# Optimization experiments

Hardware: AMD Instinct MI355X
Metric: run time of the kernel (lower is better)

The kernel has to match this reference:

```python
import jax, jax.numpy as jnp
import numpy as np

DIM = 1024
HEAD_DIM = 64
NUM_HEADS = DIM // HEAD_DIM
SCALE = HEAD_DIM ** -0.5
B, N, M = 2, 1024, 2048


def setup_inputs() -> dict:
    key = jax.random.key(0)
    ks = jax.random.split(key, 7)
    x = jax.random.normal(ks[0], (B, N, DIM), dtype=jnp.float32)
    context = jax.random.normal(ks[1], (B, M, DIM), dtype=jnp.float32)
    # query row has at least one valid key (avoids all -inf softmax rows).
    mask = jax.random.bernoulli(ks[2], 0.9, (B, N, M))
    mask = mask.at[:, :, 0].set(True)
    # Linear params (torch nn.Linear convention: y = x @ W.T + b)
    sq = (1.0 / DIM) ** 0.5
    Wq = jax.random.uniform(ks[3], (DIM, DIM), minval=-sq, maxval=sq, dtype=jnp.float32)
    Wkv = jax.random.uniform(ks[4], (2 * DIM, DIM), minval=-sq, maxval=sq, dtype=jnp.float32)
    b_kv = jax.random.uniform(ks[5], (2 * DIM,), minval=-sq, maxval=sq, dtype=jnp.float32)
    Wo = jax.random.uniform(ks[6], (DIM, DIM), minval=-sq, maxval=sq, dtype=jnp.float32)
    return {"x": x, "context": context, "mask": mask,
            "Wq": Wq, "Wkv": Wkv, "b_kv": b_kv, "Wo": Wo}


def reference(x, context, mask, Wq, Wkv, b_kv, Wo):
    b, n, c = x.shape
    m = context.shape[1]
    h, d = NUM_HEADS, HEAD_DIM
    # Q projection (no bias): [b, n, h, d] -> bhnd
    q = (x @ Wq.T).reshape(b, n, h, d).transpose(0, 2, 1, 3)
    # KV projection (with bias): [b, m, 2, h, d]
    kv = (context @ Wkv.T + b_kv).reshape(b, m, 2, h, d)
    k = kv[:, :, 0].transpose(0, 2, 1, 3)  # bhmd
    v = kv[:, :, 1].transpose(0, 2, 1, 3)  # bhmd
    # scores: bhnm, scale applied after matmul as in the original
    attn = jnp.einsum('bhnd,bhmd->bhnm', q, k) * SCALE
    attn = jnp.where(mask[:, None, :, :], attn, -jnp.inf)
    attn = jax.nn.softmax(attn, axis=-1)
    out = jnp.einsum('bhnm,bhmd->bhnd', attn, v)
    out = out.transpose(0, 2, 1, 3).reshape(b, n, h * d)
    return out @ Wo.T
```

## Files before the change

### kernel.cpp

```cpp
#include <hip/hip_runtime.h>


typedef __attribute__((ext_vector_type(8))) short short8;
typedef __attribute__((ext_vector_type(4))) short short4v;
typedef __attribute__((ext_vector_type(4))) float f32x4;
typedef __attribute__((ext_vector_type(4))) int int4v;

#define SCL2E 0.18033688011112042592f

__device__ __forceinline__ short f2bf(float f) {
  unsigned u = __float_as_uint(f);
  u += 0x7fffu + ((u >> 16) & 1u);
  return (short)(u >> 16);
}
__device__ __forceinline__ int cvt_pk_bf16(float a, float b) {
  int r;
  asm("v_cvt_pk_bf16_f32 %0, %1, %2" : "=v"(r) : "v"(a), "v"(b));
  return r;
}
__device__ __forceinline__ void gld_lds16(const void* gp, void* lp) {
  __builtin_amdgcn_global_load_lds(
      (const __attribute__((address_space(1))) unsigned int*)gp,
      (__attribute__((address_space(3))) unsigned int*)lp, 16, 0, 0);
}
__device__ __forceinline__ void sbar() {
  __builtin_amdgcn_sched_barrier(0);
  __builtin_amdgcn_s_barrier();
  __builtin_amdgcn_sched_barrier(0);
}
#define WAITVM(N) asm volatile("s_waitcnt vmcnt(" #N ")" ::: "memory")

__device__ __forceinline__ void pipesync() {
  asm volatile("s_waitcnt vmcnt(0) lgkmcnt(0)" ::: "memory");
  __builtin_amdgcn_sched_barrier(0);
  __builtin_amdgcn_s_barrier();
  __builtin_amdgcn_sched_barrier(0);
}
__device__ __forceinline__ short4v cvt4(float4 v) {
  short4v o;
  o[0] = f2bf(v.x); o[1] = f2bf(v.y); o[2] = f2bf(v.z); o[3] = f2bf(v.w);
  return o;
}
__device__ __forceinline__ size_t off64(int row, int k) {
  return ((size_t)(((row >> 6) * 32 + (k >> 5)) * 4 + ((row >> 4) & 3)) << 9) +
         (((((k >> 3) & 3) * 16 + (row & 15)) << 3) + (k & 7));
}

__global__ __launch_bounds__(256) void prep(
    const unsigned char* __restrict__ mask, unsigned long long* __restrict__ pm,
    const float* __restrict__ Wq, const float* __restrict__ Wkv,
    const float* __restrict__ Wo, const float* __restrict__ x,
    const float* __restrict__ ctx, short* __restrict__ wqb,
    short* __restrict__ wkvb, short* __restrict__ wob,
    short* __restrict__ xb, short* __restrict__ ctxb) {
  __shared__ __align__(16) short lds[64][136];
  const int row = blockIdx.x;
  const int wave = threadIdx.x >> 6, lane = threadIdx.x & 63;
  const unsigned char p8 = mask[lane * 4 + 1];
  const int p32 = ((const int*)mask)[lane * 2 + 1];
  const int shift =
      (__ballot(p8 != 0) != 0ull) ? 0 : ((__ballot(p32 != 0) != 0ull) ? 2 : 3);
  const size_t mbase = ((size_t)row * 2048) << shift;
#pragma unroll
  for (int j = 0; j < 8; j++) {
    const int c = wave * 512 + j * 64 + lane;
    const unsigned long long bits = __ballot(mask[mbase + ((size_t)c << shift)] != 0);
    if (lane == 0) pm[(size_t)row * 32 + wave * 8 + j] = bits;
  }

  const int bid = blockIdx.x;
  if (bid >= 1280) return;
  const float* src;
  short* dst;
  int cb;
  bool t64 = false;
  if (bid < 256) {
    src = x; dst = xb; cb = bid;
  } else if (bid < 768) {
    src = ctx; dst = ctxb; cb = bid - 256;
  } else if (bid < 1024) {
    src = Wkv; dst = wkvb; cb = bid - 768;
  } else if (bid < 1152) {
    src = Wq; dst = wqb; cb = bid - 1024;
  } else {
    src = Wo; dst = wob; cb = bid - 1152; t64 = true;
  }
  const int R0 = (cb >> 3) * 64, C0 = (cb & 7) * 128;
  const int t = threadIdx.x;
#pragma unroll
  for (int p = 0; p < 8; p++) {
    const int r = R0 + p * 8 + (t >> 5), c = C0 + (t & 31) * 4;
    const float4 v = *(const float4*)(src + (size_t)r * 1024 + c);
    *(short4v*)&lds[p * 8 + (t >> 5)][(t & 31) * 4] = cvt4(v);
  }
  __syncthreads();
  const int rt = t64 ? (R0 >> 6) : (R0 >> 7);
  const int f0 = t64 ? 0 : ((R0 >> 6) & 1) * 4;
  const int fl = t >> 6, q = (t >> 4) & 3, r15 = t & 15;
  const int lrow = fl * 16 + r15;
#pragma unroll
  for (int kc_l = 0; kc_l < 4; kc_l++) {
    const int kc = (C0 >> 5) + kc_l;
    const size_t base = t64 ? ((size_t)((rt * 32 + kc) * 4)) * 512
                            : ((size_t)((rt * 32 + kc) * 8 + f0)) * 512;
    const short8 vv = *(const short8*)&lds[lrow][kc_l * 32 + q * 8];
    *(short8*)(dst + base + t * 8) = vv;
  }
}

__global__ __launch_bounds__(256, 3)
void qkv_gemm(const short* __restrict__ xb, const short* __restrict__ ctxb,
              const short* __restrict__ wqb, const short* __restrict__ wkvb,
              const float* __restrict__ bias, short* __restrict__ qws,
              short* __restrict__ kws, short* __restrict__ vtws) {
  __shared__ __align__(16) short ldsA[3][4096];
  __shared__ __align__(16) short ldsB[3][4096];
  const int tid = threadIdx.x;
  const int wave = tid >> 6, lane = tid & 63;
  const int l15 = lane & 15, lg = lane >> 4;
  const int bx0 = blockIdx.x;
  const int bx = (bx0 & 7) * 80 + (bx0 >> 3);
  const bool isKV = bx < 512;
  const int rt = isKV ? (bx >> 4) : ((bx - 512) >> 3);
  const int ct = isKV ? (bx & 15) : ((bx - 512) & 7);
  const short* Amat = isKV ? ctxb : xb;
  const short* Bw = isKV ? wkvb : wqb;
  const int wr = wave >> 1, wc = wave & 1;

  f32x4 acc[4][4];
#pragma unroll
  for (int i = 0; i < 4; i++)
#pragma unroll
    for (int j = 0; j < 4; j++) acc[i][j] = (f32x4){0.f, 0.f, 0.f, 0.f};

  const short* ga0 = Amat + (size_t)rt * 131072 + wave * 512 + lane * 8;
  const short* ga1 = ga0 + 2048;
  const short* gb0 = Bw + (size_t)ct * 131072 + wave * 512 + lane * 8;
  const short* gb1 = gb0 + 2048;

  auto stage = [&](int kk, int buf) {
    const size_t koff = (size_t)kk * 4096;
    short* dA = &ldsA[buf][0];
    short* dB = &ldsB[buf][0];
    gld_lds16(ga0 + koff, dA + wave * 512);
    gld_lds16(ga1 + koff, dA + (wave + 4) * 512);
    gld_lds16(gb0 + koff, dB + wave * 512);
    gld_lds16(gb1 + koff, dB + (wave + 4) * 512);
  };
  auto compute = [&](int buf) {
    const short* sA = &ldsA[buf][0];
    const short* sB = &ldsB[buf][0];
    short8 af[4], bfr[4];
#pragma unroll
    for (int t = 0; t < 4; t++)
      af[t] = *(const short8*)&sA[((wr * 4 + t) * 64 + lane) * 8];
#pragma unroll
    for (int t = 0; t < 4; t++)
      bfr[t] = *(const short8*)&sB[((wc * 4 + t) * 64 + lane) * 8];
#pragma unroll
    for (int i = 0; i < 4; i++)
#pragma unroll
      for (int j = 0; j < 4; j++)
        acc[i][j] =
            __builtin_amdgcn_mfma_f32_16x16x32_bf16(af[i], bfr[j], acc[i][j], 0, 0, 0);
  };

  stage(0, 0);
  stage(1, 1);
  int cur = 0, nxt = 2;
  for (int i = 0; i < 30; ++i) {
    WAITVM(4);
    sbar();
    stage(i + 2, nxt);
    compute(cur);
    cur = (cur == 2) ? 0 : cur + 1;
    nxt = (nxt == 2) ? 0 : nxt + 1;
  }
  WAITVM(4);
  sbar();
  compute(cur);
  cur = (cur == 2) ? 0 : cur + 1;
  WAITVM(0);
  sbar();
  compute(cur);

#pragma unroll
  for (int i = 0; i < 4; i++)
#pragma unroll
    for (int j = 0; j < 4; j++)
#pragma unroll
      for (int r = 0; r < 4; r++) {
        const int gr = rt * 128 + wr * 64 + i * 16 + lg * 4 + r;
        const int gc = ct * 128 + wc * 64 + j * 16 + l15;
        float v = acc[i][j][r];
        if (isKV) {
          v += bias[gc];
          const int b = gr >> 11, m = gr & 2047;
          const int kv = gc >> 10, hh = (gc >> 6) & 15, d = gc & 63;
          if (kv == 0)
            kws[((((size_t)b * 16 + hh) * 2048 + m) << 6) + d] = f2bf(v);
          else {
            const int mp = (m & ~31) | (((m >> 2) & 3) << 3) |
                           (((m >> 4) & 1) << 2) | (m & 3);
            vtws[(((size_t)b * 16 + hh) * 64 + d) * 2048 + mp] = f2bf(v);
          }
        } else {
          const int b = gr >> 10, n = gr & 1023, hh = gc >> 6, d = gc & 63;
          qws[((((size_t)b * 16 + hh) * 1024 + n) << 6) + d] = f2bf(v * SCL2E);
        }
      }
}

__global__ __launch_bounds__(512, 4)
void attn_split(const short* __restrict__ Qg, const short* __restrict__ Kg,
                const short* __restrict__ Vtg,
                const unsigned int* __restrict__ pm,
                float* __restrict__ opart, float* __restrict__ lpart) {
  __shared__ __align__(16) short ldsK[2][8192];
  __shared__ __align__(16) short ldsV[2][8192];
  const int tid = threadIdx.x;
  const int w = tid >> 6, lane = tid & 63;
  const int l15 = lane & 15, lg = lane >> 4;
  const int bx = blockIdx.x;
  const int bhid = bx & 31, qt = (bx >> 5) & 7, half = bx >> 8;
  const int b = bhid >> 4, h = bhid & 15;
  const int n0 = qt * 128, m_base = half * 1024;
  const size_t bh = (size_t)b * 16 + h;
  const short* Qb = Qg + (bh * 1024 + n0) * 64;
  const short* Kb = Kg + (bh << 17);
  const short* Vb = Vtg + (bh << 17);
  const unsigned int* pmw =
      pm + ((size_t)(b * 1024 + n0 + w * 16 + l15) << 6) + (m_base >> 5);

  uint4 mku[8];
#pragma unroll
  for (int c = 0; c < 8; c++) mku[c] = *(const uint4*)(pmw + c * 4);

  auto stageKV = [&](int c, int buf) {
    const int m0 = m_base + c * 128;
    short* dK = &ldsK[buf][0];
    short* dV = &ldsV[buf][0];
#pragma unroll
    for (int ii = 0; ii < 2; ii++) {
      const int f = w * 2 + ii;
      const int t = f >> 1, ks = f & 1;
      gld_lds16(Kb + (size_t)(m0 + t * 16 + l15) * 64 + ks * 32 + lg * 8,
                dK + f * 512);
      const int vt = f >> 2, vk = f & 3;
      gld_lds16(Vb + (size_t)(vt * 16 + l15) * 2048 + (m0 + vk * 32 + lg * 8),
                dV + f * 512);
    }
  };

#pragma unroll
  for (int ii = 0; ii < 2; ii++)
    gld_lds16(Qb + (size_t)(w * 16 + l15) * 64 + ii * 32 + lg * 8,
              &ldsV[1][(w * 2 + ii) * 512]);
  stageKV(0, 0);
  pipesync();
  short8 qf[2];
#pragma unroll
  for (int ks = 0; ks < 2; ks++)
    qf[ks] = *(const short8*)&ldsV[1][((w * 2 + ks) * 64 + lane) * 8];
  asm volatile("s_waitcnt lgkmcnt(0)" ::: "memory");
  sbar();

  short8 onesf;
#pragma unroll
  for (int i = 0; i < 8; i++) onesf[i] = (short)0x3F80;

  f32x4 o[4], lacc;
#pragma unroll
  for (int ct = 0; ct < 4; ct++) o[ct] = (f32x4){0.f, 0.f, 0.f, 0.f};
  lacc = (f32x4){0.f, 0.f, 0.f, 0.f};
  const int sb = lg * 4;

  auto computeC = [&](uint4 mk, int buf) {
    const short* sK = &ldsK[buf][0];
    const short* sV = &ldsV[buf][0];
    int4v pw4[4];
#pragma unroll
    for (int h2 = 0; h2 < 2; h2++) {
      f32x4 s[4];
#pragma unroll
      for (int t2 = 0; t2 < 4; t2++) s[t2] = (f32x4){0.f, 0.f, 0.f, 0.f};
      __builtin_amdgcn_s_setprio(1);
#pragma unroll
      for (int t2 = 0; t2 < 4; t2++) {
        const int t = h2 * 4 + t2;
#pragma unroll
        for (int ks = 0; ks < 2; ks++) {
          const short8 kf = *(const short8*)&sK[((t * 2 + ks) * 64 + lane) * 8];
          s[t2] = __builtin_amdgcn_mfma_f32_16x16x32_bf16(kf, qf[ks], s[t2], 0, 0, 0);
        }
      }
      __builtin_amdgcn_s_setprio(0);
#pragma unroll
      for (int t2 = 0; t2 < 4; t2++) {
        const int t = h2 * 4 + t2;
        const unsigned int mw = ((t >> 1) == 0) ? mk.x
                              : ((t >> 1) == 1) ? mk.y
                              : ((t >> 1) == 2) ? mk.z : mk.w;
        float p[4];
#pragma unroll
        for (int r = 0; r < 4; r++) {
          const bool att = (mw >> (((t & 1) << 4) + sb + r)) & 1;
          p[r] = exp2f(att ? s[t2][r] : -1e30f);
        }
        pw4[t >> 1][(t & 1) * 2] = cvt_pk_bf16(p[0], p[1]);
        pw4[t >> 1][(t & 1) * 2 + 1] = cvt_pk_bf16(p[2], p[3]);
      }
    }
    __builtin_amdgcn_s_setprio(1);
#pragma unroll
    for (int ks2 = 0; ks2 < 4; ks2++) {
      const short8 pf = __builtin_bit_cast(short8, pw4[ks2]);
#pragma unroll
      for (int ct = 0; ct < 4; ct++) {
        const short8 vf = *(const short8*)&sV[((ct * 4 + ks2) * 64 + lane) * 8];
        o[ct] = __builtin_amdgcn_mfma_f32_16x16x32_bf16(pf, vf, o[ct], 0, 0, 0);
      }
      lacc = __builtin_amdgcn_mfma_f32_16x16x32_bf16(pf, onesf, lacc, 0, 0, 0);
    }
    __builtin_amdgcn_s_setprio(0);
  };

#pragma unroll
  for (int c = 0; c < 8; c++) {
    if (c + 1 < 8) {
      stageKV(c + 1, (c + 1) & 1);
      WAITVM(4);
    } else {
      WAITVM(0);
    }
    sbar();
    computeC(mku[c], c & 1);
    sbar();
  }

#pragma unroll
  for (int ct = 0; ct < 4; ct++)
#pragma unroll
    for (int r = 0; r < 4; r++) {
      const int n = n0 + w * 16 + lg * 4 + r;
      opart[((size_t)half << 21) + (((size_t)b * 1024 + n) << 10) + h * 64 +
            ct * 16 + l15] = o[ct][r];
    }
  if (l15 == 0) {
#pragma unroll
    for (int r = 0; r < 4; r++) {
      const int n = n0 + w * 16 + lg * 4 + r;
      lpart[((size_t)half << 15) + bh * 1024 + n] = lacc[r];
    }
  }
}

__global__ __launch_bounds__(256) void combine(
    const float* __restrict__ opart, const float* __restrict__ lpart,
    short* __restrict__ aoT) {
  const int gid = blockIdx.x * 256 + threadIdx.x;
  const int T = gid * 4;
  const int j = T & 4, r15 = (T >> 3) & 15, q = (T >> 7) & 3;
  const int f = (T >> 9) & 3, kc = (T >> 11) & 31, rt = T >> 16;
  const int row = rt * 64 + f * 16 + r15;
  const int col = kc * 32 + q * 8 + j;
  const int b = row >> 10, n = row & 1023, h = col >> 6;
  const size_t src = (((size_t)row) << 10) + col;
  const float4 o1 = *(const float4*)(opart + src);
  const float4 o2 = *(const float4*)(opart + (1u << 21) + src);
  const float l1 = lpart[(size_t)(b * 16 + h) * 1024 + n];
  const float l2 = lpart[(1u << 15) + (size_t)(b * 16 + h) * 1024 + n];
  const float inv = 1.f / fmaxf(l1 + l2, 1e-30f);
  short4v o;
  o[0] = f2bf((o1.x + o2.x) * inv); o[1] = f2bf((o1.y + o2.y) * inv);
  o[2] = f2bf((o1.z + o2.z) * inv); o[3] = f2bf((o1.w + o2.w) * inv);
  *(short4v*)(aoT + T) = o;
}

__global__ __launch_bounds__(256, 3)
void o_gemm(const short* __restrict__ aoT, const short* __restrict__ wobT,
            float* __restrict__ Of) {
  __shared__ __align__(16) short ldsA[3][4096];
  __shared__ __align__(16) short ldsB[3][4096];
  const int tid = threadIdx.x;
  const int w = tid >> 6, lane = tid & 63;
  const int l15 = lane & 15, lg = lane >> 4;
  const int bx0 = blockIdx.x;
  const int bx = (bx0 & 7) * 64 + (bx0 >> 3);
  const int rt = bx >> 4, ct = bx & 15;

  f32x4 acc[4];
#pragma unroll
  for (int j = 0; j < 4; j++) acc[j] = (f32x4){0.f, 0.f, 0.f, 0.f};

  const short* ga = aoT + (size_t)rt * 65536 + w * 512 + lane * 8;
  const short* gb = wobT + (size_t)ct * 65536 + w * 512 + lane * 8;

  auto stage = [&](int t, int buf) {
    const size_t koff = (size_t)t * 4096;
    gld_lds16(ga + koff, &ldsA[buf][0] + w * 512);
    gld_lds16(ga + koff + 2048, &ldsA[buf][0] + 2048 + w * 512);
    gld_lds16(gb + koff, &ldsB[buf][0] + w * 512);
    gld_lds16(gb + koff + 2048, &ldsB[buf][0] + 2048 + w * 512);
  };
  auto compute = [&](int buf) {
    const short* sA = &ldsA[buf][0];
    const short* sB = &ldsB[buf][0];
    const short8 af0 = *(const short8*)&sA[(w * 64 + lane) * 8];
    const short8 af1 = *(const short8*)&sA[2048 + (w * 64 + lane) * 8];
#pragma unroll
    for (int j = 0; j < 4; j++) {
      const short8 bf0 = *(const short8*)&sB[(j * 64 + lane) * 8];
      const short8 bf1 = *(const short8*)&sB[2048 + (j * 64 + lane) * 8];
      acc[j] = __builtin_amdgcn_mfma_f32_16x16x32_bf16(af0, bf0, acc[j], 0, 0, 0);
      acc[j] = __builtin_amdgcn_mfma_f32_16x16x32_bf16(af1, bf1, acc[j], 0, 0, 0);
    }
  };

  stage(0, 0);
  stage(1, 1);
#pragma unroll
  for (int i = 0; i < 14; ++i) {
    WAITVM(4);
    sbar();
    stage(i + 2, (i + 2) % 3);
    compute(i % 3);
  }
  WAITVM(4);
  sbar();
  compute(14 % 3);
  WAITVM(0);
  sbar();
  compute(15 % 3);

#pragma unroll
  for (int j = 0; j < 4; j++)
#pragma unroll
    for (int r = 0; r < 4; r++) {
      const int gr = rt * 64 + w * 16 + lg * 4 + r;
      const int gc = ct * 64 + j * 16 + l15;
      Of[(size_t)gr * 1024 + gc] = acc[j][r];
    }
}

extern "C" void kernel_launch(void* const* d_in, const int* in_sizes, int n_in,
                              void* d_out, int out_size, void* d_ws, size_t ws_size,
                              hipStream_t stream) {
  const float* x   = (const float*)d_in[0];
  const float* ctx = (const float*)d_in[1];
  const unsigned char* mask = (const unsigned char*)d_in[2];
  const float* Wq  = (const float*)d_in[3];
  const float* Wkv = (const float*)d_in[4];
  const float* bkv = (const float*)d_in[5];
  const float* Wo  = (const float*)d_in[6];
  float* out = (float*)d_out;

  char* wsb = (char*)d_ws;
  short* qws  = (short*)(wsb);
  short* kws  = (short*)(wsb + (4u << 20));
  short* vtws = (short*)(wsb + (12u << 20));
  short* wqb  = (short*)(wsb + (20u << 20));
  short* wkvb = (short*)(wsb + (22u << 20));
  short* wob  = (short*)(wsb + (26u << 20));
  unsigned long long* pmws = (unsigned long long*)(wsb + (28u << 20));
  float* opart = (float*)(wsb + (29u << 20));
  float* lpart = (float*)(wsb + (45u << 20));
  short* xb   = (short*)(wsb + (29u << 20));
  short* ctxb = (short*)(wsb + (33u << 20));
  short* ao = (short*)(wsb + (20u << 20));

  prep<<<2048, 256, 0, stream>>>(mask, pmws, Wq, Wkv, Wo, x, ctx,
                                 wqb, wkvb, wob, xb, ctxb);
  qkv_gemm<<<640, 256, 0, stream>>>(xb, ctxb, wqb, wkvb, bkv, qws, kws, vtws);
  attn_split<<<512, 512, 0, stream>>>(qws, kws, vtws, (const unsigned int*)pmws,
                                      opart, lpart);
  combine<<<2048, 256, 0, stream>>>(opart, lpart, ao);
  o_gemm<<<512, 256, 0, stream>>>(ao, wob, out);
}
```

Measured before the change: 202.4 us.

## Fuse split-attention combine into output projection GEMM prologue

Removes the separate combine kernel and has o_gemm read the two fp32 partial outputs directly, sum them, scale by the inverse softmax denominator per head, convert to bf16 and write into LDS for the A operand. The pipeline now prefetches A tiles into registers alongside the async B loads. This drops one kernel launch and the bf16 intermediate round trip through memory. In exchange the GEMM reads fp32 A data (more bytes per tile, and each A tile is re-read by all 16 column tiles) and uses more registers, which may lower occupancy.

Measured after the change: 228.3 us. 12.8% more time.

```diff
diff --git a/kernel.cpp b/kernel.cpp
--- a/kernel.cpp
+++ b/kernel.cpp
@@ -29,6 +29,7 @@
   __builtin_amdgcn_sched_barrier(0);
 }
 #define WAITVM(N) asm volatile("s_waitcnt vmcnt(" #N ")" ::: "memory")
+#define WAITLGKM0 asm volatile("s_waitcnt lgkmcnt(0)" ::: "memory")
 
 __device__ __forceinline__ void pipesync() {
   asm volatile("s_waitcnt vmcnt(0) lgkmcnt(0)" ::: "memory");
@@ -40,10 +41,6 @@
   short4v o;
   o[0] = f2bf(v.x); o[1] = f2bf(v.y); o[2] = f2bf(v.z); o[3] = f2bf(v.w);
   return o;
-}
-__device__ __forceinline__ size_t off64(int row, int k) {
-  return ((size_t)(((row >> 6) * 32 + (k >> 5)) * 4 + ((row >> 4) & 3)) << 9) +
-         (((((k >> 3) & 3) * 16 + (row & 15)) << 3) + (k & 7));
 }
 
 __global__ __launch_bounds__(256) void prep(
@@ -262,7 +259,7 @@
 #pragma unroll
   for (int ks = 0; ks < 2; ks++)
     qf[ks] = *(const short8*)&ldsV[1][((w * 2 + ks) * 64 + lane) * 8];
-  asm volatile("s_waitcnt lgkmcnt(0)" ::: "memory");
+  WAITLGKM0;
   sbar();
 
   short8 onesf;
@@ -355,31 +352,9 @@
   }
 }
 
-__global__ __launch_bounds__(256) void combine(
-    const float* __restrict__ opart, const float* __restrict__ lpart,
-    short* __restrict__ aoT) {
-  const int gid = blockIdx.x * 256 + threadIdx.x;
-  const int T = gid * 4;
-  const int j = T & 4, r15 = (T >> 3) & 15, q = (T >> 7) & 3;
-  const int f = (T >> 9) & 3, kc = (T >> 11) & 31, rt = T >> 16;
-  const int row = rt * 64 + f * 16 + r15;
-  const int col = kc * 32 + q * 8 + j;
-  const int b = row >> 10, n = row & 1023, h = col >> 6;
-  const size_t src = (((size_t)row) << 10) + col;
-  const float4 o1 = *(const float4*)(opart + src);
-  const float4 o2 = *(const float4*)(opart + (1u << 21) + src);
-  const float l1 = lpart[(size_t)(b * 16 + h) * 1024 + n];
-  const float l2 = lpart[(1u << 15) + (size_t)(b * 16 + h) * 1024 + n];
-  const float inv = 1.f / fmaxf(l1 + l2, 1e-30f);
-  short4v o;
-  o[0] = f2bf((o1.x + o2.x) * inv); o[1] = f2bf((o1.y + o2.y) * inv);
-  o[2] = f2bf((o1.z + o2.z) * inv); o[3] = f2bf((o1.w + o2.w) * inv);
-  *(short4v*)(aoT + T) = o;
-}
-
 __global__ __launch_bounds__(256, 3)
-void o_gemm(const short* __restrict__ aoT, const short* __restrict__ wobT,
-            float* __restrict__ Of) {
+void o_gemm(const float* __restrict__ opart, const float* __restrict__ lpart,
+            const short* __restrict__ wobT, float* __restrict__ Of) {
   __shared__ __align__(16) short ldsA[3][4096];
   __shared__ __align__(16) short ldsB[3][4096];
   const int tid = threadIdx.x;
@@ -389,19 +364,53 @@
   const int bx = (bx0 & 7) * 64 + (bx0 >> 3);
   const int rt = bx >> 4, ct = bx & 15;
 
+  const int arow = rt * 64 + (tid >> 6) * 16 + (tid & 15);
+  const int kq8 = ((tid >> 4) & 3) * 8;
+  const int ab = arow >> 10, an = arow & 1023;
+  const float* srcA = opart + ((size_t)arow << 10);
+
+  float inv[16];
+#pragma unroll
+  for (int h = 0; h < 16; h++) {
+    const float l1 = lpart[(size_t)(ab * 16 + h) * 1024 + an];
+    const float l2 = lpart[(1u << 15) + (size_t)(ab * 16 + h) * 1024 + an];
+    inv[h] = 1.f / fmaxf(l1 + l2, 1e-30f);
+  }
+
   f32x4 acc[4];
 #pragma unroll
   for (int j = 0; j < 4; j++) acc[j] = (f32x4){0.f, 0.f, 0.f, 0.f};
 
-  const short* ga = aoT + (size_t)rt * 65536 + w * 512 + lane * 8;
   const short* gb = wobT + (size_t)ct * 65536 + w * 512 + lane * 8;
 
-  auto stage = [&](int t, int buf) {
+  float4 rg[2][8];
+  auto loadA = [&](float4* r, int t) {
+    const float* p = srcA + t * 64 + kq8;
+    r[0] = *(const float4*)(p);
+    r[1] = *(const float4*)(p + 4);
+    r[2] = *(const float4*)(p + 32);
+    r[3] = *(const float4*)(p + 36);
+    const float* p2 = p + (1u << 21);
+    r[4] = *(const float4*)(p2);
+    r[5] = *(const float4*)(p2 + 4);
+    r[6] = *(const float4*)(p2 + 32);
+    r[7] = *(const float4*)(p2 + 36);
+  };
+  auto stageB = [&](int t, int buf) {
     const size_t koff = (size_t)t * 4096;
-    gld_lds16(ga + koff, &ldsA[buf][0] + w * 512);
-    gld_lds16(ga + koff + 2048, &ldsA[buf][0] + 2048 + w * 512);
     gld_lds16(gb + koff, &ldsB[buf][0] + w * 512);
     gld_lds16(gb + koff + 2048, &ldsB[buf][0] + 2048 + w * 512);
+  };
+  auto writeA = [&](const float4* r, int t, int buf) {
+    const float iv = inv[t];
+    const float4 q0 = (r[0] + r[4]) * iv;
+    const float4 q1 = (r[1] + r[5]) * iv;
+    const float4 q2 = (r[2] + r[6]) * iv;
+    const float4 q3 = (r[3] + r[7]) * iv;
+    *(short4v*)&ldsA[buf][tid * 8] = cvt4(q0);
+    *(short4v*)&ldsA[buf][tid * 8 + 4] = cvt4(q1);
+    *(short4v*)&ldsA[buf][2048 + tid * 8] = cvt4(q2);
+    *(short4v*)&ldsA[buf][2048 + tid * 8 + 4] = cvt4(q3);
   };
   auto compute = [&](int buf) {
     const short* sA = &ldsA[buf][0];
@@ -417,21 +426,32 @@
     }
   };
 
-  stage(0, 0);
-  stage(1, 1);
-#pragma unroll
-  for (int i = 0; i < 14; ++i) {
-    WAITVM(4);
+  loadA(rg[0], 0);
+  stageB(0, 0);
+  loadA(rg[1], 1);
+  stageB(1, 1);
+  WAITVM(10);
+  writeA(rg[0], 0, 0);
+  WAITLGKM0;
+
+#pragma unroll
+  for (int i = 0; i < 16; i++) {
     sbar();
-    stage(i + 2, (i + 2) % 3);
+    if (i + 2 < 16) {
+      loadA(rg[i & 1], i + 2);
+      stageB(i + 2, (i + 2) % 3);
+    }
     compute(i % 3);
-  }
-  WAITVM(4);
-  sbar();
-  compute(14 % 3);
-  WAITVM(0);
-  sbar();
-  compute(15 % 3);
+    if (i + 1 < 16) {
+      if (i + 2 < 16) {
+        WAITVM(10);
+      } else {
+        WAITVM(0);
+      }
+      writeA(rg[(i + 1) & 1], i + 1, (i + 1) % 3);
+    }
+    WAITLGKM0;
+  }
 
 #pragma unroll
   for (int j = 0; j < 4; j++)
@@ -467,13 +487,11 @@
   float* lpart = (float*)(wsb + (45u << 20));
   short* xb   = (short*)(wsb + (29u << 20));
   short* ctxb = (short*)(wsb + (33u << 20));
-  short* ao = (short*)(wsb + (20u << 20));
 
   prep<<<2048, 256, 0, stream>>>(mask, pmws, Wq, Wkv, Wo, x, ctx,
                                  wqb, wkvb, wob, xb, ctxb);
   qkv_gemm<<<640, 256, 0, stream>>>(xb, ctxb, wqb, wkvb, bkv, qws, kws, vtws);
   attn_split<<<512, 512, 0, stream>>>(qws, kws, vtws, (const unsigned int*)pmws,
                                       opart, lpart);
-  combine<<<2048, 256, 0, stream>>>(opart, lpart, ao);
-  o_gemm<<<512, 256, 0, stream>>>(ao, wob, out);
-}
+  o_gemm<<<512, 256, 0, stream>>>(opart, lpart, wob, out);
+}
```
